# Kernel optimization log

Hardware: AMD Instinct MI355X
Metric: run time of the kernel (lower is better)

The kernel has to match this reference:

```python
import jax, jax.numpy as jnp
import numpy as np

S = 8192          # tokens
D = 4096          # model_dim
E = 64            # num_experts
CAP_FACTOR = 1.0
MIN_CAPACITY = 8
CAPACITY = max(int(np.ceil(S / E * CAP_FACTOR)), MIN_CAPACITY)  # = 128


def setup_inputs() -> dict:
    key = jax.random.key(0)
    kx, kw = jax.random.split(key)
    x = jax.random.normal(kx, (S, D), dtype=jnp.float32)
    # torch Linear weight [out_features, in_features] = [E, D]
    wg = jax.random.normal(kw, (E, D), dtype=jnp.float32) * (1.0 / np.sqrt(D))
    return {"x": x, "wg": wg}


def reference(x, wg):
    # logits = wg(input_fp32): [s, e]
    logits = jnp.einsum('sd,ed->se', x.astype(jnp.float32), wg)
    gates = jax.nn.softmax(logits, axis=1)                     # [s, e]

    # top-1 expert per token (argmax of softmax == argmax of logits)
    indices1_s = jnp.argmax(gates, axis=1)                     # [s]
    mask1 = jax.nn.one_hot(indices1_s, E, dtype=jnp.int32)     # [s, e]
    exp_counts = jnp.sum(mask1, axis=0)                        # [e]

    # load-balancing aux loss (uses pre-capacity mask, as in torch)
    me = jnp.mean(gates, axis=0)
    ce = jnp.mean(mask1.astype(jnp.float32), axis=0)
    l_aux = jnp.sum(me * ce) * E

    # capacity truncation: keep first CAPACITY routed tokens per expert
    # (equivalent to mask1 * scatter(topk(mask1, capacity, dim=0)) when
    #  use_rts=False, since topk over 0/1 tie-breaks by lowest index)
    loc0 = jnp.cumsum(mask1, axis=0) - 1                       # [s, e]
    mask1 = mask1 * (loc0 < CAPACITY).astype(jnp.int32)

    # slot positions within each expert's capacity buffer
    locations1 = jnp.cumsum(mask1, axis=0) - 1                 # [s, e]
    locations1_s = jnp.sum(locations1 * mask1, axis=1)         # [s]

    mask1_float = mask1.astype(jnp.float32)
    gates = gates * mask1_float                                # [s, e]
    locations1_sc = jax.nn.one_hot(locations1_s, CAPACITY, dtype=jnp.float32)  # [s, c]

    combine_weights = jnp.einsum('se,sc->sec', gates, locations1_sc)  # [s, e, c]
    dispatch_mask = combine_weights.astype(bool)
    return (l_aux, combine_weights, dispatch_mask, exp_counts)
```

## Files before the change

### kernel.cpp

```cpp
#include <hip/hip_runtime.h>
#include <cstdint>

#define TS 8192
#define TD 4096
#define TE 64
#define TCAP 128
#define KS 16
#define KB (TD/KS)
#define KC 32
#define TB 256
#define NTB (TS/TB)

static constexpr size_t SEC = (size_t)TS * TE * TCAP;

typedef float f32x4 __attribute__((ext_vector_type(4)));

__global__ __launch_bounds__(256) void fill_half(f32x4* __restrict__ out4)
{
    const f32x4 z = {0.f, 0.f, 0.f, 0.f};
    const long base = 16777216L;
    const long c0 = base + (long)blockIdx.x * 2048;
    #pragma unroll
    for (int j = 0; j < 8; ++j)
        __builtin_nontemporal_store(z, &out4[c0 + (long)j * 256 + threadIdx.x]);
    if (blockIdx.x == 0 && threadIdx.x < 16)
        __builtin_nontemporal_store(z, &out4[base + 16777216L + threadIdx.x]);
}

__global__ __launch_bounds__(512, 4) void gemm_fill(
    const float* __restrict__ x, const float* __restrict__ wg,
    float* __restrict__ part, f32x4* __restrict__ out4,
    float* __restrict__ out)
{
    __shared__ float xs[KC][260];
    __shared__ float wsh[KC][68];

    const int tid = threadIdx.x;
    const int bid = blockIdx.x;
    const int tb  = bid & (NTB - 1);
    const int ks  = bid >> 5;
    const int tok0 = tb * TB;
    const int tx = tid & 15;
    const int ty = tid >> 4;
    const int kq_s  = tid & 7;
    const int row_s = tid >> 3;
    const long fill0 = (long)bid * 32768;
    const f32x4 z4 = {0.f, 0.f, 0.f, 0.f};

    float acc[8][4];
    #pragma unroll
    for (int i = 0; i < 8; ++i)
        #pragma unroll
        for (int j = 0; j < 4; ++j) acc[i][j] = 0.f;

    f32x4 rx[4], rw;
    {
        const int k0 = ks * KB;
        #pragma unroll
        for (int r = 0; r < 4; ++r)
            rx[r] = __builtin_nontemporal_load(reinterpret_cast<const f32x4*>(
                &x[(size_t)(tok0 + r * 64 + row_s) * TD + k0 + kq_s * 4]));
        rw = *reinterpret_cast<const f32x4*>(&wg[(size_t)row_s * TD + k0 + kq_s * 4]);
    }

    for (int it = 0; it < KB / KC; ++it) {
        #pragma unroll
        for (int r = 0; r < 4; ++r) {
            const int t = r * 64 + row_s;
            xs[kq_s*4+0][t] = rx[r].x; xs[kq_s*4+1][t] = rx[r].y;
            xs[kq_s*4+2][t] = rx[r].z; xs[kq_s*4+3][t] = rx[r].w;
        }
        wsh[kq_s*4+0][row_s] = rw.x; wsh[kq_s*4+1][row_s] = rw.y;
        wsh[kq_s*4+2][row_s] = rw.z; wsh[kq_s*4+3][row_s] = rw.w;
        __syncthreads();
        if (it + 1 < KB / KC) {
            const int k0 = ks * KB + (it + 1) * KC;
            #pragma unroll
            for (int r = 0; r < 4; ++r)
                rx[r] = __builtin_nontemporal_load(reinterpret_cast<const f32x4*>(
                    &x[(size_t)(tok0 + r * 64 + row_s) * TD + k0 + kq_s * 4]));
            rw = *reinterpret_cast<const f32x4*>(&wg[(size_t)row_s * TD + k0 + kq_s * 4]);
        }
        #pragma unroll
        for (int k = 0; k < KC; ++k) {
            if (k < 8) {
                __builtin_nontemporal_store(z4,
                    &out4[fill0 + (long)it * 4096 + k * 512 + tid]);
            }
            const f32x4 a0 = *reinterpret_cast<const f32x4*>(&xs[k][ty * 8]);
            const f32x4 a1 = *reinterpret_cast<const f32x4*>(&xs[k][ty * 8 + 4]);
            const f32x4 b  = *reinterpret_cast<const f32x4*>(&wsh[k][tx * 4]);
            acc[0][0] = fmaf(a0.x, b.x, acc[0][0]);
            acc[0][1] = fmaf(a0.x, b.y, acc[0][1]);
            acc[0][2] = fmaf(a0.x, b.z, acc[0][2]);
            acc[0][3] = fmaf(a0.x, b.w, acc[0][3]);
            acc[1][0] = fmaf(a0.y, b.x, acc[1][0]);
            acc[1][1] = fmaf(a0.y, b.y, acc[1][1]);
            acc[1][2] = fmaf(a0.y, b.z, acc[1][2]);
            acc[1][3] = fmaf(a0.y, b.w, acc[1][3]);
            acc[2][0] = fmaf(a0.z, b.x, acc[2][0]);
            acc[2][1] = fmaf(a0.z, b.y, acc[2][1]);
            acc[2][2] = fmaf(a0.z, b.z, acc[2][2]);
            acc[2][3] = fmaf(a0.z, b.w, acc[2][3]);
            acc[3][0] = fmaf(a0.w, b.x, acc[3][0]);
            acc[3][1] = fmaf(a0.w, b.y, acc[3][1]);
            acc[3][2] = fmaf(a0.w, b.z, acc[3][2]);
            acc[3][3] = fmaf(a0.w, b.w, acc[3][3]);
            acc[4][0] = fmaf(a1.x, b.x, acc[4][0]);
            acc[4][1] = fmaf(a1.x, b.y, acc[4][1]);
            acc[4][2] = fmaf(a1.x, b.z, acc[4][2]);
            acc[4][3] = fmaf(a1.x, b.w, acc[4][3]);
            acc[5][0] = fmaf(a1.y, b.x, acc[5][0]);
            acc[5][1] = fmaf(a1.y, b.y, acc[5][1]);
            acc[5][2] = fmaf(a1.y, b.z, acc[5][2]);
            acc[5][3] = fmaf(a1.y, b.w, acc[5][3]);
            acc[6][0] = fmaf(a1.z, b.x, acc[6][0]);
            acc[6][1] = fmaf(a1.z, b.y, acc[6][1]);
            acc[6][2] = fmaf(a1.z, b.z, acc[6][2]);
            acc[6][3] = fmaf(a1.z, b.w, acc[6][3]);
            acc[7][0] = fmaf(a1.w, b.x, acc[7][0]);
            acc[7][1] = fmaf(a1.w, b.y, acc[7][1]);
            acc[7][2] = fmaf(a1.w, b.z, acc[7][2]);
            acc[7][3] = fmaf(a1.w, b.w, acc[7][3]);
        }
        __syncthreads();
    }
    if (bid == 0 && tid == 0) out[2 * SEC + 64] = 0.f;
    #pragma unroll
    for (int i = 0; i < 8; ++i) {
        const int t = tok0 + ty * 8 + i;
        f32x4 v;
        v.x = acc[i][0]; v.y = acc[i][1]; v.z = acc[i][2]; v.w = acc[i][3];
        *reinterpret_cast<f32x4*>(&part[((size_t)ks * TS + t) * TE + tx * 4]) = v;
    }
}

__global__ __launch_bounds__(256) void softmax_argmax(
    const float* __restrict__ part, int* __restrict__ eidx,
    float* __restrict__ gtop, float* __restrict__ partial_me)
{
    __shared__ float cs[4][64];
    const int tid = threadIdx.x;
    const int tx = tid & 15;
    const int ty = tid >> 4;
    const int s = blockIdx.x * 16 + ty;

    float p[4] = {0.f, 0.f, 0.f, 0.f};
    #pragma unroll
    for (int ks = 0; ks < KS; ++ks) {
        const f32x4 v = *reinterpret_cast<const f32x4*>(
            &part[((size_t)ks * TS + s) * TE + tx * 4]);
        p[0] += v.x; p[1] += v.y; p[2] += v.z; p[3] += v.w;
    }

    float lm = fmaxf(fmaxf(p[0], p[1]), fmaxf(p[2], p[3]));
    #pragma unroll
    for (int mask = 1; mask <= 8; mask <<= 1)
        lm = fmaxf(lm, __shfl_xor(lm, mask));
    float ep[4]; float ls = 0.f;
    #pragma unroll
    for (int j = 0; j < 4; ++j) { ep[j] = __expf(p[j] - lm); ls += ep[j]; }
    #pragma unroll
    for (int mask = 1; mask <= 8; mask <<= 1)
        ls += __shfl_xor(ls, mask);
    const float invZ = 1.0f / ls;

    float bv = p[0]; int bi = tx * 4;
    #pragma unroll
    for (int j = 1; j < 4; ++j)
        if (p[j] > bv) { bv = p[j]; bi = tx * 4 + j; }
    #pragma unroll
    for (int mask = 1; mask <= 8; mask <<= 1) {
        const float ov = __shfl_xor(bv, mask);
        const int   oi = __shfl_xor(bi, mask);
        if (ov > bv || (ov == bv && oi < bi)) { bv = ov; bi = oi; }
    }
    if (tx == 0) { eidx[s] = bi; gtop[s] = invZ; }

    float colsum[4];
    #pragma unroll
    for (int j = 0; j < 4; ++j) colsum[j] = ep[j] * invZ;
    #pragma unroll
    for (int j = 0; j < 4; ++j) {
        colsum[j] += __shfl_xor(colsum[j], 16);
        colsum[j] += __shfl_xor(colsum[j], 32);
    }
    const int wave = tid >> 6;
    const int lane = tid & 63;
    if (lane < 16) {
        #pragma unroll
        for (int j = 0; j < 4; ++j) cs[wave][lane * 4 + j] = colsum[j];
    }
    __syncthreads();
    if (tid < 64) {
        partial_me[(size_t)blockIdx.x * 64 + tid] =
            cs[0][tid] + cs[1][tid] + cs[2][tid] + cs[3][tid];
    }
}

__global__ __launch_bounds__(1024) void rank_scatter_laux(
    const int* __restrict__ eidx, const float* __restrict__ gtop,
    const float* __restrict__ partial_me, float* __restrict__ out)
{
    const int e = blockIdx.x;
    const int tid = threadIdx.x;
    const int wave = tid >> 6;
    const int lane = tid & 63;
    __shared__ int wave_tot[16];
    __shared__ float red[8];

    int ev[8];
    #pragma unroll
    for (int r = 0; r < 8; ++r) ev[r] = eidx[r * 1024 + tid];

    int running = 0;
    #pragma unroll
    for (int r = 0; r < 8; ++r) {
        const bool m = (ev[r] == e);
        const unsigned long long b = __ballot(m);
        if (lane == 0) wave_tot[wave] = __popcll(b);
        __syncthreads();
        int off = running;
        #pragma unroll
        for (int w = 0; w < 16; ++w) if (w < wave) off += wave_tot[w];
        const int rank = off + __popcll(b & ((1ull << lane) - 1ull));
        if (m && rank < TCAP) {
            const int s = r * 1024 + tid;
            const size_t base = 1 + ((size_t)s * TE + e) * TCAP + (size_t)rank;
            out[base] = gtop[s];
            out[base + SEC] = 1.0f;
        }
        int tot = 0;
        #pragma unroll
        for (int w = 0; w < 16; ++w) tot += wave_tot[w];
        running += tot;
        __syncthreads();
    }
    if (tid == 0) out[1 + 2 * SEC + e] = (float)running;

    float v = (tid < 512) ? partial_me[(size_t)tid * 64 + e] : 0.f;
    #pragma unroll
    for (int mask = 32; mask >= 1; mask >>= 1) v += __shfl_xor(v, mask);
    if (lane == 0 && wave < 8) red[wave] = v;
    __syncthreads();
    if (tid == 0) {
        float ms = 0.f;
        #pragma unroll
        for (int w = 0; w < 8; ++w) ms += red[w];
        const float me = ms * (1.0f / TS);
        const float ce = (float)running * (1.0f / TS);
        atomicAdd(out, me * ce * (float)TE);
    }
}

extern "C" void kernel_launch(void* const* d_in, const int* in_sizes, int n_in,
                              void* d_out, int out_size, void* d_ws, size_t ws_size,
                              hipStream_t stream) {
    const float* x  = (const float*)d_in[0];
    const float* wg = (const float*)d_in[1];
    float* out = (float*)d_out;

    float* part       = (float*)d_ws;
    int*   eidx       = (int*)(part + (size_t)KS * TS * TE);
    float* gtop       = (float*)(eidx + TS);
    float* partial_me = gtop + TS;

    hipLaunchKernelGGL(fill_half, dim3(8192), dim3(256), 0, stream,
                       (f32x4*)out);
    hipLaunchKernelGGL(gemm_fill, dim3(512), dim3(512), 0, stream,
                       x, wg, part, (f32x4*)out, out);
    hipLaunchKernelGGL(softmax_argmax, dim3(512), dim3(256), 0, stream,
                       part, eidx, gtop, partial_me);
    hipLaunchKernelGGL(rank_scatter_laux, dim3(64), dim3(1024), 0, stream,
                       eidx, gtop, partial_me, out);
}
```

Before: 154.9 us.

## Fuse output zero-fill into GEMM kernel using dedicated fill warps

Removes the separate fill_half kernel and the fill stores interleaved in the GEMM loop. Instead, 256 extra threads per block (block size 768) zero-fill the whole output buffer while 512 threads do the logits GEMM. The fill threads join the block barriers so the two roles stay in lockstep, and the zeroing of the output tail and l_aux slot moves to these threads. This saves a launch and overlaps the memory-bound fill with compute. In exchange, dropping the launch bound of 4 blocks per SM may cut occupancy or raise register pressure, and the barrier count must match between branches.

```diff
diff --git a/kernel.cpp b/kernel.cpp
--- a/kernel.cpp
+++ b/kernel.cpp
@@ -15,19 +15,7 @@
 
 typedef float f32x4 __attribute__((ext_vector_type(4)));
 
-__global__ __launch_bounds__(256) void fill_half(f32x4* __restrict__ out4)
-{
-    const f32x4 z = {0.f, 0.f, 0.f, 0.f};
-    const long base = 16777216L;
-    const long c0 = base + (long)blockIdx.x * 2048;
-    #pragma unroll
-    for (int j = 0; j < 8; ++j)
-        __builtin_nontemporal_store(z, &out4[c0 + (long)j * 256 + threadIdx.x]);
-    if (blockIdx.x == 0 && threadIdx.x < 16)
-        __builtin_nontemporal_store(z, &out4[base + 16777216L + threadIdx.x]);
-}
-
-__global__ __launch_bounds__(512, 4) void gemm_fill(
+__global__ __launch_bounds__(768) void gemm_fill_fused(
     const float* __restrict__ x, const float* __restrict__ wg,
     float* __restrict__ part, f32x4* __restrict__ out4,
     float* __restrict__ out)
@@ -37,101 +25,112 @@
 
     const int tid = threadIdx.x;
     const int bid = blockIdx.x;
-    const int tb  = bid & (NTB - 1);
-    const int ks  = bid >> 5;
-    const int tok0 = tb * TB;
-    const int tx = tid & 15;
-    const int ty = tid >> 4;
-    const int kq_s  = tid & 7;
-    const int row_s = tid >> 3;
-    const long fill0 = (long)bid * 32768;
-    const f32x4 z4 = {0.f, 0.f, 0.f, 0.f};
-
-    float acc[8][4];
-    #pragma unroll
-    for (int i = 0; i < 8; ++i)
-        #pragma unroll
-        for (int j = 0; j < 4; ++j) acc[i][j] = 0.f;
-
-    f32x4 rx[4], rw;
-    {
-        const int k0 = ks * KB;
-        #pragma unroll
-        for (int r = 0; r < 4; ++r)
-            rx[r] = __builtin_nontemporal_load(reinterpret_cast<const f32x4*>(
-                &x[(size_t)(tok0 + r * 64 + row_s) * TD + k0 + kq_s * 4]));
-        rw = *reinterpret_cast<const f32x4*>(&wg[(size_t)row_s * TD + k0 + kq_s * 4]);
-    }
-
-    for (int it = 0; it < KB / KC; ++it) {
-        #pragma unroll
-        for (int r = 0; r < 4; ++r) {
-            const int t = r * 64 + row_s;
-            xs[kq_s*4+0][t] = rx[r].x; xs[kq_s*4+1][t] = rx[r].y;
-            xs[kq_s*4+2][t] = rx[r].z; xs[kq_s*4+3][t] = rx[r].w;
-        }
-        wsh[kq_s*4+0][row_s] = rw.x; wsh[kq_s*4+1][row_s] = rw.y;
-        wsh[kq_s*4+2][row_s] = rw.z; wsh[kq_s*4+3][row_s] = rw.w;
-        __syncthreads();
-        if (it + 1 < KB / KC) {
-            const int k0 = ks * KB + (it + 1) * KC;
+
+    if (tid < 512) {
+        const int tb  = bid & (NTB - 1);
+        const int ks  = bid >> 5;
+        const int tok0 = tb * TB;
+        const int tx = tid & 15;
+        const int ty = tid >> 4;
+        const int kq_s  = tid & 7;
+        const int row_s = tid >> 3;
+
+        float acc[8][4];
+        #pragma unroll
+        for (int i = 0; i < 8; ++i)
+            #pragma unroll
+            for (int j = 0; j < 4; ++j) acc[i][j] = 0.f;
+
+        f32x4 rx[4], rw;
+        {
+            const int k0 = ks * KB;
             #pragma unroll
             for (int r = 0; r < 4; ++r)
                 rx[r] = __builtin_nontemporal_load(reinterpret_cast<const f32x4*>(
                     &x[(size_t)(tok0 + r * 64 + row_s) * TD + k0 + kq_s * 4]));
             rw = *reinterpret_cast<const f32x4*>(&wg[(size_t)row_s * TD + k0 + kq_s * 4]);
         }
-        #pragma unroll
-        for (int k = 0; k < KC; ++k) {
-            if (k < 8) {
-                __builtin_nontemporal_store(z4,
-                    &out4[fill0 + (long)it * 4096 + k * 512 + tid]);
-            }
-            const f32x4 a0 = *reinterpret_cast<const f32x4*>(&xs[k][ty * 8]);
-            const f32x4 a1 = *reinterpret_cast<const f32x4*>(&xs[k][ty * 8 + 4]);
-            const f32x4 b  = *reinterpret_cast<const f32x4*>(&wsh[k][tx * 4]);
-            acc[0][0] = fmaf(a0.x, b.x, acc[0][0]);
-            acc[0][1] = fmaf(a0.x, b.y, acc[0][1]);
-            acc[0][2] = fmaf(a0.x, b.z, acc[0][2]);
-            acc[0][3] = fmaf(a0.x, b.w, acc[0][3]);
-            acc[1][0] = fmaf(a0.y, b.x, acc[1][0]);
-            acc[1][1] = fmaf(a0.y, b.y, acc[1][1]);
-            acc[1][2] = fmaf(a0.y, b.z, acc[1][2]);
-            acc[1][3] = fmaf(a0.y, b.w, acc[1][3]);
-            acc[2][0] = fmaf(a0.z, b.x, acc[2][0]);
-            acc[2][1] = fmaf(a0.z, b.y, acc[2][1]);
-            acc[2][2] = fmaf(a0.z, b.z, acc[2][2]);
-            acc[2][3] = fmaf(a0.z, b.w, acc[2][3]);
-            acc[3][0] = fmaf(a0.w, b.x, acc[3][0]);
-            acc[3][1] = fmaf(a0.w, b.y, acc[3][1]);
-            acc[3][2] = fmaf(a0.w, b.z, acc[3][2]);
-            acc[3][3] = fmaf(a0.w, b.w, acc[3][3]);
-            acc[4][0] = fmaf(a1.x, b.x, acc[4][0]);
-            acc[4][1] = fmaf(a1.x, b.y, acc[4][1]);
-            acc[4][2] = fmaf(a1.x, b.z, acc[4][2]);
-            acc[4][3] = fmaf(a1.x, b.w, acc[4][3]);
-            acc[5][0] = fmaf(a1.y, b.x, acc[5][0]);
-            acc[5][1] = fmaf(a1.y, b.y, acc[5][1]);
-            acc[5][2] = fmaf(a1.y, b.z, acc[5][2]);
-            acc[5][3] = fmaf(a1.y, b.w, acc[5][3]);
-            acc[6][0] = fmaf(a1.z, b.x, acc[6][0]);
-            acc[6][1] = fmaf(a1.z, b.y, acc[6][1]);
-            acc[6][2] = fmaf(a1.z, b.z, acc[6][2]);
-            acc[6][3] = fmaf(a1.z, b.w, acc[6][3]);
-            acc[7][0] = fmaf(a1.w, b.x, acc[7][0]);
-            acc[7][1] = fmaf(a1.w, b.y, acc[7][1]);
-            acc[7][2] = fmaf(a1.w, b.z, acc[7][2]);
-            acc[7][3] = fmaf(a1.w, b.w, acc[7][3]);
-        }
-        __syncthreads();
-    }
-    if (bid == 0 && tid == 0) out[2 * SEC + 64] = 0.f;
-    #pragma unroll
-    for (int i = 0; i < 8; ++i) {
-        const int t = tok0 + ty * 8 + i;
-        f32x4 v;
-        v.x = acc[i][0]; v.y = acc[i][1]; v.z = acc[i][2]; v.w = acc[i][3];
-        *reinterpret_cast<f32x4*>(&part[((size_t)ks * TS + t) * TE + tx * 4]) = v;
+
+        for (int it = 0; it < KB / KC; ++it) {
+            #pragma unroll
+            for (int r = 0; r < 4; ++r) {
+                const int t = r * 64 + row_s;
+                xs[kq_s*4+0][t] = rx[r].x; xs[kq_s*4+1][t] = rx[r].y;
+                xs[kq_s*4+2][t] = rx[r].z; xs[kq_s*4+3][t] = rx[r].w;
+            }
+            wsh[kq_s*4+0][row_s] = rw.x; wsh[kq_s*4+1][row_s] = rw.y;
+            wsh[kq_s*4+2][row_s] = rw.z; wsh[kq_s*4+3][row_s] = rw.w;
+            __syncthreads();
+            if (it + 1 < KB / KC) {
+                const int k0 = ks * KB + (it + 1) * KC;
+                #pragma unroll
+                for (int r = 0; r < 4; ++r)
+                    rx[r] = __builtin_nontemporal_load(reinterpret_cast<const f32x4*>(
+                        &x[(size_t)(tok0 + r * 64 + row_s) * TD + k0 + kq_s * 4]));
+                rw = *reinterpret_cast<const f32x4*>(&wg[(size_t)row_s * TD + k0 + kq_s * 4]);
+            }
+            #pragma unroll
+            for (int k = 0; k < KC; ++k) {
+                const f32x4 a0 = *reinterpret_cast<const f32x4*>(&xs[k][ty * 8]);
+                const f32x4 a1 = *reinterpret_cast<const f32x4*>(&xs[k][ty * 8 + 4]);
+                const f32x4 b  = *reinterpret_cast<const f32x4*>(&wsh[k][tx * 4]);
+                acc[0][0] = fmaf(a0.x, b.x, acc[0][0]);
+                acc[0][1] = fmaf(a0.x, b.y, acc[0][1]);
+                acc[0][2] = fmaf(a0.x, b.z, acc[0][2]);
+                acc[0][3] = fmaf(a0.x, b.w, acc[0][3]);
+                acc[1][0] = fmaf(a0.y, b.x, acc[1][0]);
+                acc[1][1] = fmaf(a0.y, b.y, acc[1][1]);
+                acc[1][2] = fmaf(a0.y, b.z, acc[1][2]);
+                acc[1][3] = fmaf(a0.y, b.w, acc[1][3]);
+                acc[2][0] = fmaf(a0.z, b.x, acc[2][0]);
+                acc[2][1] = fmaf(a0.z, b.y, acc[2][1]);
+                acc[2][2] = fmaf(a0.z, b.z, acc[2][2]);
+                acc[2][3] = fmaf(a0.z, b.w, acc[2][3]);
+                acc[3][0] = fmaf(a0.w, b.x, acc[3][0]);
+                acc[3][1] = fmaf(a0.w, b.y, acc[3][1]);
+                acc[3][2] = fmaf(a0.w, b.z, acc[3][2]);
+                acc[3][3] = fmaf(a0.w, b.w, acc[3][3]);
+                acc[4][0] = fmaf(a1.x, b.x, acc[4][0]);
+                acc[4][1] = fmaf(a1.x, b.y, acc[4][1]);
+                acc[4][2] = fmaf(a1.x, b.z, acc[4][2]);
+                acc[4][3] = fmaf(a1.x, b.w, acc[4][3]);
+                acc[5][0] = fmaf(a1.y, b.x, acc[5][0]);
+                acc[5][1] = fmaf(a1.y, b.y, acc[5][1]);
+                acc[5][2] = fmaf(a1.y, b.z, acc[5][2]);
+                acc[5][3] = fmaf(a1.y, b.w, acc[5][3]);
+                acc[6][0] = fmaf(a1.z, b.x, acc[6][0]);
+                acc[6][1] = fmaf(a1.z, b.y, acc[6][1]);
+                acc[6][2] = fmaf(a1.z, b.z, acc[6][2]);
+                acc[6][3] = fmaf(a1.z, b.w, acc[6][3]);
+                acc[7][0] = fmaf(a1.w, b.x, acc[7][0]);
+                acc[7][1] = fmaf(a1.w, b.y, acc[7][1]);
+                acc[7][2] = fmaf(a1.w, b.z, acc[7][2]);
+                acc[7][3] = fmaf(a1.w, b.w, acc[7][3]);
+            }
+            __syncthreads();
+        }
+        #pragma unroll
+        for (int i = 0; i < 8; ++i) {
+            const int t = tok0 + ty * 8 + i;
+            f32x4 v;
+            v.x = acc[i][0]; v.y = acc[i][1]; v.z = acc[i][2]; v.w = acc[i][3];
+            *reinterpret_cast<f32x4*>(&part[((size_t)ks * TS + t) * TE + tx * 4]) = v;
+        }
+    } else {
+        const int ft = tid - 512;
+        const long base = (long)bid * 65536;
+        const f32x4 z = {0.f, 0.f, 0.f, 0.f};
+        for (int it = 0; it < 8; ++it) {
+            #pragma unroll
+            for (int seg = 0; seg < 2; ++seg) {
+                #pragma unroll
+                for (int j = 0; j < 16; ++j)
+                    __builtin_nontemporal_store(z,
+                        &out4[base + (long)it * 8192 + seg * 4096 + j * 256 + ft]);
+                __syncthreads();
+            }
+        }
+        if (bid == 0 && ft < 65) out[2 * SEC + ft] = 0.f;
     }
 }
 
@@ -265,9 +264,7 @@
     float* gtop       = (float*)(eidx + TS);
     float* partial_me = gtop + TS;
 
-    hipLaunchKernelGGL(fill_half, dim3(8192), dim3(256), 0, stream,
-                       (f32x4*)out);
-    hipLaunchKernelGGL(gemm_fill, dim3(512), dim3(512), 0, stream,
+    hipLaunchKernelGGL(gemm_fill_fused, dim3(512), dim3(768), 0, stream,
                        x, wg, part, (f32x4*)out, out);
     hipLaunchKernelGGL(softmax_argmax, dim3(512), dim3(256), 0, stream,
                        part, eidx, gtop, partial_me);
```

Result: slower. 166.1 us (+7.3%).
